# Kernel tuning notes

Measured on AMD Instinct MI355X. Metric: run time of the kernel, lower is better.

## Reference

```python
import jax, jax.numpy as jnp
import numpy as np
from jax import lax

T_STEPS = 10       # fixed unroll length in forward (range(10))
TASK = 16          # params['task_size']
FEAT = 256         # input_size - task_size
VOCAB = 128        # params['vocab_size']
SH = 512           # sender_hidden_size
RH = 512           # receiver_hidden_size
ND = 10            # num_digits
B = 16384          # batch_size


def _gru_step(h, x, Wih, Whh, bih, bhh):
    # PyTorch GRU/GRUCell equations. Wih: [3H, In], Whh: [3H, H]
    gi = x @ Wih.T + bih
    gh = h @ Whh.T + bhh
    ir, iz, inn = jnp.split(gi, 3, axis=-1)
    hr, hz, hn = jnp.split(gh, 3, axis=-1)
    r = jax.nn.sigmoid(ir + hr)
    z = jax.nn.sigmoid(iz + hz)
    n = jnp.tanh(inn + r * hn)
    return (1.0 - z) * n + z * h


def setup_inputs() -> dict:
    key = jax.random.key(0)
    ks = jax.random.split(key, 16)
    s = 0.05
    x = jax.random.normal(ks[0], (B, TASK + FEAT), jnp.float32)
    u = jax.random.uniform(ks[1], (T_STEPS, B, VOCAB), jnp.float32, 1e-6, 1.0 - 1e-6)
    gumbel = -jnp.log(-jnp.log(u))  # standard Gumbel noise, fixed for determinism
    inp = {
        "x": x,
        "gumbel": gumbel,
        "W_in": jax.random.normal(ks[2], (SH, FEAT), jnp.float32) * s,
        "b_in": jnp.zeros((SH,), jnp.float32),
        "Wih_s": jax.random.normal(ks[3], (3 * SH, VOCAB), jnp.float32) * s,
        "Whh_s": jax.random.normal(ks[4], (3 * SH, SH), jnp.float32) * s,
        "bih_s": jnp.zeros((3 * SH,), jnp.float32),
        "bhh_s": jnp.zeros((3 * SH,), jnp.float32),
        "W_sp": jax.random.normal(ks[5], (VOCAB, SH), jnp.float32) * s,
        "b_sp": jnp.zeros((VOCAB,), jnp.float32),
        "Wih_r": jax.random.normal(ks[6], (3 * RH, VOCAB), jnp.float32) * s,
        "Whh_r": jax.random.normal(ks[7], (3 * RH, RH), jnp.float32) * s,
        "bih_r": jnp.zeros((3 * RH,), jnp.float32),
        "bhh_r": jnp.zeros((3 * RH,), jnp.float32),
        "W_c": jax.random.normal(ks[8], (ND, RH + TASK), jnp.float32) * s,
        "b_c": jnp.zeros((ND,), jnp.float32),
    }
    return inp


def _forward(x, gumbel, W_in, b_in, Wih_s, Whh_s, bih_s, bhh_s, W_sp, b_sp,
             Wih_r, Whh_r, bih_r, bhh_r, W_c, b_c):
    feats = x[:, TASK:]
    task = x[:, :TASK]
    h0 = jnp.tanh(feats @ W_in.T + b_in)                      # [B, SH]
    inp0 = jnp.zeros((x.shape[0], VOCAB), x.dtype)

    def sender_step(carry, g):
        h, w = carry
        h = _gru_step(h, w, Wih_s, Whh_s, bih_s, bhh_s)
        logits = h @ W_sp.T + b_sp
        y_soft = jax.nn.softmax(logits + g, axis=-1)          # gumbel_softmax, tau=1
        onehot = jax.nn.one_hot(jnp.argmax(y_soft, axis=-1), VOCAB, dtype=y_soft.dtype)
        y = onehot + y_soft - lax.stop_gradient(y_soft)       # hard straight-through
        return (h, lax.stop_gradient(y)), y                   # input_word = y.detach()

    (_, _), output_words = lax.scan(sender_step, (h0, inp0), gumbel)  # [10, B, V]

    # cumulative stop-token masking: once argmax==0 at step i-1, zero all steps >= i
    words = jnp.argmax(output_words, axis=2)                  # [10, B]
    nz = (words != 0).astype(output_words.dtype)
    alive = jnp.concatenate(
        [jnp.ones((1, words.shape[1]), output_words.dtype), jnp.cumprod(nz[:-1], axis=0)],
        axis=0)                                               # [10, B]
    masked = output_words * alive[:, :, None]

    # receiver GRU, zero initial hidden, return final hidden
    hr0 = jnp.zeros((x.shape[0], RH), x.dtype)

    def recv_step(h, w):
        h = _gru_step(h, w, Wih_r, Whh_r, bih_r, bhh_r)
        return h, None

    h_n, _ = lax.scan(recv_step, hr0, masked)                 # [B, RH]
    score = jnp.concatenate([h_n, task], axis=1) @ W_c.T + b_c  # [B, ND]
    return score


def reference(x, gumbel, W_in, b_in, Wih_s, Whh_s, bih_s, bhh_s, W_sp, b_sp,
              Wih_r, Whh_r, bih_r, bhh_r, W_c, b_c):
    return _forward(x, gumbel, W_in, b_in, Wih_s, Whh_s, bih_s, bhh_s, W_sp, b_sp,
                    Wih_r, Whh_r, bih_r, bhh_r, W_c, b_c)
```

## Files before the change

### kernel.cpp

```cpp
#include <hip/hip_runtime.h>
#include <math.h>

#define NB 16384
#define NT 10

typedef _Float16 f16;
typedef f16 f16x8 __attribute__((ext_vector_type(8)));
typedef f16 f16x4 __attribute__((ext_vector_type(4)));
typedef float f32x4 __attribute__((ext_vector_type(4)));

__device__ __forceinline__ float sigm(float v) { return 1.0f / (1.0f + expf(-v)); }
__device__ __forceinline__ float sigm_fast(float v) {
    return __builtin_amdgcn_rcpf(1.0f + __expf(-v));
}
__device__ __forceinline__ float tanh_fast(float v) {
    return 1.0f - 2.0f * __builtin_amdgcn_rcpf(1.0f + __expf(2.0f * v));
}

__device__ __forceinline__ void async_cp16(const f16* g, f16* l) {
    __builtin_amdgcn_global_load_lds(
        (const __attribute__((address_space(1))) unsigned int*)g,
        (__attribute__((address_space(3))) unsigned int*)l, 16, 0, 0);
}

__global__ __launch_bounds__(256) void h0_kernel(
    const float* __restrict__ x, const float* __restrict__ W,
    const float* __restrict__ bias, f16* __restrict__ h_hi, f16* __restrict__ h_lo)
{
    __shared__ __align__(16) float As[32][128];
    __shared__ __align__(16) float Ws[32][64];
    const int t = threadIdx.x;
    const int tx = t & 15, ty = t >> 4;
    const int mBase = blockIdx.x * 128, nBase = blockIdx.y * 64;
    const int kq = (t & 7) * 4, r8 = t >> 3;

    float4 acc[8];
    #pragma unroll
    for (int mi = 0; mi < 8; ++mi) acc[mi] = make_float4(0.f, 0.f, 0.f, 0.f);

    const float* aPtr = x + (size_t)(mBase + r8) * 272 + 16 + kq;
    const float* wPtr = W + (size_t)(nBase + r8) * 256 + kq;

    for (int kb = 0; kb < 8; ++kb) {
        const int k0 = kb * 32;
        __syncthreads();
        #pragma unroll
        for (int i = 0; i < 4; ++i) {
            float4 v = *(const float4*)(aPtr + (size_t)(i * 32) * 272 + k0);
            const int row = r8 + i * 32;
            const float vv[4] = {v.x, v.y, v.z, v.w};
            #pragma unroll
            for (int j = 0; j < 4; ++j) As[kq + j][row ^ ((kq + j) & 28)] = vv[j];
        }
        #pragma unroll
        for (int i = 0; i < 2; ++i) {
            float4 v = *(const float4*)(wPtr + (size_t)(i * 32) * 256 + k0);
            const int row = r8 + i * 32;
            const float vv[4] = {v.x, v.y, v.z, v.w};
            #pragma unroll
            for (int j = 0; j < 4; ++j) Ws[kq + j][row ^ ((kq + j) & 28)] = vv[j];
        }
        __syncthreads();
        #pragma unroll 8
        for (int k = 0; k < 32; ++k) {
            const int s = k & 28;
            float4 a0 = *(const float4*)&As[k][(ty * 8) ^ s];
            float4 a1 = *(const float4*)&As[k][((ty * 8) + 4) ^ s];
            float4 bb = *(const float4*)&Ws[k][(tx * 4) ^ s];
            const float am[8] = {a0.x, a0.y, a0.z, a0.w, a1.x, a1.y, a1.z, a1.w};
            #pragma unroll
            for (int mi = 0; mi < 8; ++mi) {
                acc[mi].x += am[mi] * bb.x; acc[mi].y += am[mi] * bb.y;
                acc[mi].z += am[mi] * bb.z; acc[mi].w += am[mi] * bb.w;
            }
        }
    }
    const int j0 = nBase + tx * 4;
    const int kg = j0 >> 3, jo = j0 & 7;
    const float4 b4 = *(const float4*)&bias[j0];
    #pragma unroll
    for (int mi = 0; mi < 8; ++mi) {
        const int row = mBase + ty * 8 + mi;
        float o[4];
        o[0] = tanhf(acc[mi].x + b4.x); o[1] = tanhf(acc[mi].y + b4.y);
        o[2] = tanhf(acc[mi].z + b4.z); o[3] = tanhf(acc[mi].w + b4.w);
        f16x4 hi4, lo4;
        #pragma unroll
        for (int c = 0; c < 4; ++c) {
            f16 hv = (f16)o[c];
            hi4[c] = hv;
            lo4[c] = (f16)(o[c] - (float)hv);
        }
        *(f16x4*)&h_hi[((size_t)kg * NB + row) * 8 + jo] = hi4;
        *(f16x4*)&h_lo[((size_t)kg * NB + row) * 8 + jo] = lo4;
    }
}

__global__ __launch_bounds__(256) void wsplit_kernel(
    const float* __restrict__ W, f16* __restrict__ whi, f16* __restrict__ wlo, int rows)
{
    const int u = blockIdx.x * 256 + threadIdx.x;
    const int kg = u / rows, row = u - kg * rows;
    const float* s = W + (size_t)row * 512 + kg * 8;
    f16x8 hi8, lo8;
    #pragma unroll
    for (int i = 0; i < 8; ++i) {
        float v = s[i];
        f16 hv = (f16)v;
        hi8[i] = hv;
        lo8[i] = (f16)(v - (float)hv);
    }
    *(f16x8*)&whi[(size_t)u * 8] = hi8;
    *(f16x8*)&wlo[(size_t)u * 8] = lo8;
}

__global__ __launch_bounds__(256) void wihT_kernel(
    const float* __restrict__ Wih, float* __restrict__ WihT)
{
    const int u = blockIdx.x * 256 + threadIdx.x;
    const int w = u / 1536, c = u - w * 1536;
    WihT[u] = Wih[(size_t)c * 128 + w];
}

#define INIT_SP() { \
    _Pragma("unroll") \
    for (int i = 0; i < NST; ++i) { \
        const int u = i * 256 + t; \
        const f16* src; \
        if (PURE) { \
            if (u < 512) { \
                src = hc_hi + ((size_t)(u >> 7) * NB + m0 + (u & 127)) * 8; \
            } else { \
                const int w = u - 512; \
                src = w_hi + ((size_t)((w >> 6) & 3) * 1536 + (w >> 8) * 512 + n0 + (w & 63)) * 8; \
            } \
        } else { \
            if (u < 1024) { \
                const int v = u & 511; \
                const f16* hp = (u < 512) ? hc_hi : hc_lo; \
                src = hp + ((size_t)(v >> 7) * NB + m0 + (v & 127)) * 8; \
            } else { \
                const int v = u - 1024; \
                const f16* wp = (v < 768) ? w_hi : w_lo; \
                const int w = (v < 768) ? v : v - 768; \
                src = wp + ((size_t)((w >> 6) & 3) * 1536 + (w >> 8) * 512 + n0 + (w & 63)) * 8; \
            } \
        } \
        sp[i] = src; \
    } \
}
#define STAGE(buf_) { \
    f16* lb_ = lds + ((size_t)(buf_) * UNITS + wbase) * 8; \
    _Pragma("unroll") \
    for (int i = 0; i < NST; ++i) { \
        async_cp16(sp[i], lb_ + (size_t)i * 256 * 8); \
        sp[i] += (i < HCNT) ? (size_t)NB * 32 : (size_t)49152; \
    } \
}

template <int HZERO, int PURE>
__global__ __launch_bounds__(256, 2) void fused_gru(
    const f16* __restrict__ hc_hi, const f16* __restrict__ hc_lo,
    f16* __restrict__ hn_hi, f16* __restrict__ hn_lo,
    const f16* __restrict__ w_hi, const f16* __restrict__ w_lo,
    const float* __restrict__ WihT,
    const float* __restrict__ bih, const float* __restrict__ bhh,
    const int* __restrict__ wsel)
{
    constexpr int UNITS = PURE ? 1280 : 2560;
    constexpr int NST = PURE ? 5 : 10;
    constexpr int HCNT = PURE ? 2 : 4;
    __shared__ __align__(16) f16 lds[2 * UNITS * 8];
    const int t = threadIdx.x;
    const int lane = t & 63, wave = t >> 6;
    const int wm = wave >> 1, wn = wave & 1;
    const int nid = (blockIdx.x & 7) * (NB / 128 * 8 / 8) + (blockIdx.x >> 3);
    const int m0 = (nid >> 3) * 128;
    const int n0 = (nid & 7) * 64;
    const int wbase = t & 192;

    const f32x4 z4 = {0.f, 0.f, 0.f, 0.f};
    f32x4 acc[3][4][2];
    #pragma unroll
    for (int g = 0; g < 3; ++g)
        #pragma unroll
        for (int mi = 0; mi < 4; ++mi)
            #pragma unroll
            for (int ni = 0; ni < 2; ++ni) acc[g][mi][ni] = z4;

    if (!HZERO) {
        const int asel = ((lane >> 4) << 7) + wm * 64 + (lane & 15);
        const int bsel = ((lane >> 4) << 6) + wn * 32 + (lane & 15);
        constexpr int B0 = PURE ? 512 : 1024;

        const f16* sp[NST];
        INIT_SP();
        STAGE(0);
        asm volatile("s_waitcnt vmcnt(0)" ::: "memory");
        __syncthreads();

        for (int kb = 0; kb < 16; ++kb) {
            if (kb < 15) STAGE((kb + 1) & 1);

            const f16* lb = lds + (size_t)(kb & 1) * UNITS * 8;
            f16x8 ah[4], al[4];
            #pragma unroll
            for (int mi = 0; mi < 4; ++mi) {
                ah[mi] = *(const f16x8*)&lb[(size_t)(asel + mi * 16) * 8];
                if (!PURE) al[mi] = *(const f16x8*)&lb[(size_t)(512 + asel + mi * 16) * 8];
            }
            #pragma unroll
            for (int g = 0; g < 3; ++g) {
                f16x8 bh[2], bl[2];
                #pragma unroll
                for (int ni = 0; ni < 2; ++ni) {
                    bh[ni] = *(const f16x8*)&lb[(size_t)(B0 + g * 256 + bsel + ni * 16) * 8];
                    if (!PURE) bl[ni] = *(const f16x8*)&lb[(size_t)(1792 + g * 256 + bsel + ni * 16) * 8];
                }
                #pragma unroll
                for (int mi = 0; mi < 4; ++mi)
                    #pragma unroll
                    for (int ni = 0; ni < 2; ++ni) {
                        acc[g][mi][ni] = __builtin_amdgcn_mfma_f32_16x16x32_f16(ah[mi], bh[ni], acc[g][mi][ni], 0, 0, 0);
                        if (!PURE) {
                            acc[g][mi][ni] = __builtin_amdgcn_mfma_f32_16x16x32_f16(ah[mi], bl[ni], acc[g][mi][ni], 0, 0, 0);
                            acc[g][mi][ni] = __builtin_amdgcn_mfma_f32_16x16x32_f16(al[mi], bh[ni], acc[g][mi][ni], 0, 0, 0);
                        }
                    }
            }
            __syncthreads();
        }
    }

    const int colb = n0 + wn * 32 + (lane & 15);
    const int rowb = m0 + wm * 64 + ((lane >> 4) << 2);
    int wd[16];
    #pragma unroll
    for (int mi = 0; mi < 4; ++mi)
        #pragma unroll
        for (int j = 0; j < 4; ++j)
            wd[mi * 4 + j] = wsel ? wsel[rowb + mi * 16 + j] : -1;

    #pragma unroll
    for (int ni = 0; ni < 2; ++ni) {
        const int col = colb + ni * 16;
        const float b_r = bih[col], b_z = bih[512 + col], b_n = bih[1024 + col];
        const float c_r = bhh[col], c_z = bhh[512 + col], c_n = bhh[1024 + col];
        const size_t cbase = (size_t)(col >> 3) * NB * 8 + (col & 7);
        #pragma unroll
        for (int mi = 0; mi < 4; ++mi) {
            #pragma unroll
            for (int j = 0; j < 4; ++j) {
                const int r = rowb + mi * 16 + j;
                const int word = wd[mi * 4 + j];
                float wir = 0.f, wiz = 0.f, win = 0.f;
                if (word >= 0) {
                    const float* wt = WihT + (size_t)word * 1536 + col;
                    wir = wt[0]; wiz = wt[512]; win = wt[1024];
                }
                const size_t idx = cbase + (size_t)r * 8;
                float hold = 0.f;
                if (!HZERO) {
                    hold = (float)hc_hi[idx];
                    if (!PURE) hold += (float)hc_lo[idx];
                }
                const float ra = wir + b_r + acc[0][mi][ni][j] + c_r;
                const float za = wiz + b_z + acc[1][mi][ni][j] + c_z;
                const float rr = PURE ? sigm_fast(ra) : sigm(ra);
                const float zz = PURE ? sigm_fast(za) : sigm(za);
                const float na = win + b_n + rr * (acc[2][mi][ni][j] + c_n);
                const float nn = PURE ? tanh_fast(na) : tanhf(na);
                const float hv = (1.f - zz) * nn + zz * hold;
                const f16 hh = (f16)hv;
                hn_hi[idx] = hh;
                if (!PURE) hn_lo[idx] = (f16)(hv - (float)hh);
            }
        }
    }
}

__global__ __launch_bounds__(256, 2) void argmax_mfma(
    const f16* __restrict__ h_hi, const f16* __restrict__ h_lo,
    const f16* __restrict__ wsp_hi, const f16* __restrict__ wsp_lo,
    const float* __restrict__ bsp, const float* __restrict__ gum,
    int* __restrict__ wout)
{
    __shared__ __align__(16) f16 lds[2 * 1536 * 8];
    const int t = threadIdx.x;
    const int lane = t & 63, wave = t >> 6;
    const int mBase = blockIdx.x * 64;

    const f32x4 z4 = {0.f, 0.f, 0.f, 0.f};
    f32x4 acc[8];
    #pragma unroll
    for (int nf = 0; nf < 8; ++nf) acc[nf] = z4;

    const f16* sp[6];
    sp[0] = h_hi   + ((size_t)(t >> 6) * NB + mBase + (t & 63)) * 8;
    sp[1] = h_lo   + ((size_t)(t >> 6) * NB + mBase + (t & 63)) * 8;
    sp[2] = wsp_hi + ((size_t)(t >> 7) * 128 + (t & 127)) * 8;
    sp[3] = wsp_hi + ((size_t)(2 + (t >> 7)) * 128 + (t & 127)) * 8;
    sp[4] = wsp_lo + ((size_t)(t >> 7) * 128 + (t & 127)) * 8;
    sp[5] = wsp_lo + ((size_t)(2 + (t >> 7)) * 128 + (t & 127)) * 8;

    f16x8 st[6];
    #pragma unroll
    for (int i = 0; i < 6; ++i) {
        st[i] = *(const f16x8*)sp[i];
        sp[i] += (i < 2) ? (size_t)NB * 32 : (size_t)4096;
    }

    const int aselU = (lane >> 4) * 64 + wave * 16 + (lane & 15);
    const int bselU = 512 + (lane >> 4) * 128 + (lane & 15);

    for (int kb = 0; kb < 16; ++kb) {
        f16* lb = lds + (size_t)(kb & 1) * 1536 * 8;
        #pragma unroll
        for (int i = 0; i < 6; ++i)
            *(f16x8*)&lb[(size_t)(i * 256 + t) * 8] = st[i];
        __syncthreads();
        if (kb < 15) {
            #pragma unroll
            for (int i = 0; i < 6; ++i) {
                st[i] = *(const f16x8*)sp[i];
                sp[i] += (i < 2) ? (size_t)NB * 32 : (size_t)4096;
            }
        }

        f16x8 ah = *(const f16x8*)&lb[(size_t)aselU * 8];
        f16x8 al = *(const f16x8*)&lb[(size_t)(256 + aselU) * 8];
        #pragma unroll
        for (int nf = 0; nf < 8; ++nf) {
            f16x8 bh = *(const f16x8*)&lb[(size_t)(bselU + nf * 16) * 8];
            f16x8 bl = *(const f16x8*)&lb[(size_t)(512 + bselU + nf * 16) * 8];
            acc[nf] = __builtin_amdgcn_mfma_f32_16x16x32_f16(ah, bh, acc[nf], 0, 0, 0);
            acc[nf] = __builtin_amdgcn_mfma_f32_16x16x32_f16(ah, bl, acc[nf], 0, 0, 0);
            acc[nf] = __builtin_amdgcn_mfma_f32_16x16x32_f16(al, bh, acc[nf], 0, 0, 0);
        }
    }

    float bv[4];
    int bi[4];
    #pragma unroll
    for (int j = 0; j < 4; ++j) { bv[j] = -1e30f; bi[j] = 0; }
    const int rw0 = mBase + wave * 16 + ((lane >> 4) << 2);
    #pragma unroll
    for (int nf = 0; nf < 8; ++nf) {
        const int col = (lane & 15) + nf * 16;
        const float bb = bsp[col];
        #pragma unroll
        for (int j = 0; j < 4; ++j) {
            const float v = acc[nf][j] + bb + gum[(size_t)(rw0 + j) * 128 + col];
            if (v > bv[j] || (v == bv[j] && col < bi[j])) { bv[j] = v; bi[j] = col; }
        }
    }
    #pragma unroll
    for (int j = 0; j < 4; ++j) {
        #pragma unroll
        for (int off = 1; off <= 8; off <<= 1) {
            const float ov = __shfl_xor(bv[j], off, 64);
            const int oi = __shfl_xor(bi[j], off, 64);
            if (ov > bv[j] || (ov == bv[j] && oi < bi[j])) { bv[j] = ov; bi[j] = oi; }
        }
        if ((lane & 15) == 0) wout[rw0 + j] = bi[j];
    }
}

__global__ __launch_bounds__(256) void eff_kernel(
    const int* __restrict__ words, int* __restrict__ eff)
{
    const int b = blockIdx.x * 256 + threadIdx.x;
    int alive = 1;
    #pragma unroll
    for (int t = 0; t < NT; ++t) {
        const int w = words[(size_t)t * NB + b];
        eff[(size_t)t * NB + b] = alive ? w : -1;
        alive = alive & (w != 0);
    }
}

__global__ __launch_bounds__(256) void score_kernel(
    const f16* __restrict__ h_hi,
    const float* __restrict__ x, const float* __restrict__ Wc,
    const float* __restrict__ bc, float* __restrict__ out)
{
    __shared__ float Wcs[10][528];
    const int t = threadIdx.x;
    for (int q = t; q < 1320; q += 256)
        *(float4*)&(((float*)Wcs)[q * 4]) = *(const float4*)&Wc[q * 4];
    __syncthreads();

    const int row = blockIdx.x * 256 + t;
    float acc[10];
    #pragma unroll
    for (int d = 0; d < 10; ++d) acc[d] = 0.f;

    for (int kg = 0; kg < 64; ++kg) {
        f16x8 vh = *(const f16x8*)&h_hi[((size_t)kg * NB + row) * 8];
        #pragma unroll
        for (int i = 0; i < 8; ++i) {
            const float v = (float)vh[i];
            #pragma unroll
            for (int d = 0; d < 10; ++d) acc[d] += v * Wcs[d][kg * 8 + i];
        }
    }
    #pragma unroll
    for (int j = 0; j < 16; ++j) {
        const float tv = x[(size_t)row * 272 + j];
        #pragma unroll
        for (int d = 0; d < 10; ++d) acc[d] += tv * Wcs[d][512 + j];
    }
    #pragma unroll
    for (int d = 0; d < 10; ++d) out[(size_t)row * 10 + d] = acc[d] + bc[d];
}

extern "C" void kernel_launch(void* const* d_in, const int* in_sizes, int n_in,
                              void* d_out, int out_size, void* d_ws, size_t ws_size,
                              hipStream_t stream) {
    const float* x      = (const float*)d_in[0];
    const float* gumbel = (const float*)d_in[1];
    const float* W_in   = (const float*)d_in[2];
    const float* b_in   = (const float*)d_in[3];
    const float* Wih_s  = (const float*)d_in[4];
    const float* Whh_s  = (const float*)d_in[5];
    const float* bih_s  = (const float*)d_in[6];
    const float* bhh_s  = (const float*)d_in[7];
    const float* W_sp   = (const float*)d_in[8];
    const float* b_sp   = (const float*)d_in[9];
    const float* Wih_r  = (const float*)d_in[10];
    const float* Whh_r  = (const float*)d_in[11];
    const float* bih_r  = (const float*)d_in[12];
    const float* bhh_r  = (const float*)d_in[13];
    const float* W_c    = (const float*)d_in[14];
    const float* b_c    = (const float*)d_in[15];
    float* out = (float*)d_out;

    char* base = (char*)d_ws;
    f16* S_hi[2], *S_lo[2];
    S_hi[0] = (f16*)(base);
    S_lo[0] = (f16*)(base + 16777216);
    S_hi[1] = (f16*)(base + 33554432);
    S_lo[1] = (f16*)(base + 50331648);
    f16* R0 = (f16*)(base);
    f16* R1 = (f16*)(base + 16777216);
    f16* ws_s_hi = (f16*)(base + 67108864);
    f16* ws_s_lo = (f16*)(base + 68681728);
    f16* ws_r_hi = (f16*)(base + 70254592);
    f16* ws_r_lo = (f16*)(base + 71827456);
    float* wihT_s = (float*)(base + 73400320);
    float* wihT_r = (float*)(base + 74186752);
    int* words   = (int*)(base + 74973184);
    int* eff     = (int*)(base + 75628544);
    f16* wsp_hi  = (f16*)(base + 76283904);
    f16* wsp_lo  = (f16*)(base + 76414976);

    const dim3 blk(256);
    const dim3 gFus(NB / 128 * 8);

    wsplit_kernel<<<dim3(384), blk, 0, stream>>>(Whh_s, ws_s_hi, ws_s_lo, 1536);
    wsplit_kernel<<<dim3(384), blk, 0, stream>>>(Whh_r, ws_r_hi, ws_r_lo, 1536);
    wsplit_kernel<<<dim3(32), blk, 0, stream>>>(W_sp, wsp_hi, wsp_lo, 128);
    wihT_kernel<<<dim3(768), blk, 0, stream>>>(Wih_s, wihT_s);
    wihT_kernel<<<dim3(768), blk, 0, stream>>>(Wih_r, wihT_r);

    h0_kernel<<<dim3(NB / 128, 8), blk, 0, stream>>>(x, W_in, b_in, S_hi[0], S_lo[0]);
    int cur = 0;

    for (int t = 0; t < NT; ++t) {
        const int* wprev = (t == 0) ? (const int*)nullptr : (words + (size_t)(t - 1) * NB);
        const int nxt = cur ^ 1;
        fused_gru<0, 0><<<gFus, blk, 0, stream>>>(
            S_hi[cur], S_lo[cur], S_hi[nxt], S_lo[nxt],
            ws_s_hi, ws_s_lo, wihT_s, bih_s, bhh_s, wprev);
        cur = nxt;
        argmax_mfma<<<dim3(NB / 64), blk, 0, stream>>>(
            S_hi[cur], S_lo[cur], wsp_hi, wsp_lo,
            b_sp, gumbel + (size_t)t * NB * 128, words + (size_t)t * NB);
    }
    eff_kernel<<<dim3(NB / 256), blk, 0, stream>>>(words, eff);

    fused_gru<1, 1><<<gFus, blk, 0, stream>>>(
        R1, R1, R0, R0, ws_r_hi, ws_r_lo, wihT_r, bih_r, bhh_r, eff);
    for (int t = 1; t < NT; ++t) {
        f16* rin  = (t & 1) ? R0 : R1;
        f16* rout = (t & 1) ? R1 : R0;
        fused_gru<0, 1><<<gFus, blk, 0, stream>>>(
            rin, rin, rout, rout, ws_r_hi, ws_r_lo, wihT_r, bih_r, bhh_r,
            eff + (size_t)t * NB);
    }

    score_kernel<<<dim3(NB / 256), blk, 0, stream>>>(R1, x, W_c, b_c, out);
}
```

Baseline: 1.516 ms.

## Move h0 projection to split-fp16 MFMA and use faster sender activations

Replaces the scalar fp32 FMA GEMM for the initial hidden state with an MFMA kernel. Both the input features and W_in are first split into hi/lo fp16 parts in new preprocessing kernels, and the product uses three MFMA terms to keep near-fp32 accuracy. It also swaps the sender GRU's accurate expf/tanhf for __expf-based sigmoid and tanh. The extra split kernels add memory traffic and launches, and the faster transcendentals may slightly change argmax decisions.

New measurement: 1.460 ms. 3.7% less time.

```diff
diff --git a/kernel.cpp b/kernel.cpp
--- a/kernel.cpp
+++ b/kernel.cpp
@@ -9,7 +9,8 @@
 typedef f16 f16x4 __attribute__((ext_vector_type(4)));
 typedef float f32x4 __attribute__((ext_vector_type(4)));
 
-__device__ __forceinline__ float sigm(float v) { return 1.0f / (1.0f + expf(-v)); }
+__device__ __forceinline__ float sigm_mid(float v) { return 1.0f / (1.0f + __expf(-v)); }
+__device__ __forceinline__ float tanh_mid(float v) { return 1.0f - 2.0f / (1.0f + __expf(2.0f * v)); }
 __device__ __forceinline__ float sigm_fast(float v) {
     return __builtin_amdgcn_rcpf(1.0f + __expf(-v));
 }
@@ -23,85 +24,13 @@
         (__attribute__((address_space(3))) unsigned int*)l, 16, 0, 0);
 }
 
-__global__ __launch_bounds__(256) void h0_kernel(
-    const float* __restrict__ x, const float* __restrict__ W,
-    const float* __restrict__ bias, f16* __restrict__ h_hi, f16* __restrict__ h_lo)
-{
-    __shared__ __align__(16) float As[32][128];
-    __shared__ __align__(16) float Ws[32][64];
-    const int t = threadIdx.x;
-    const int tx = t & 15, ty = t >> 4;
-    const int mBase = blockIdx.x * 128, nBase = blockIdx.y * 64;
-    const int kq = (t & 7) * 4, r8 = t >> 3;
-
-    float4 acc[8];
-    #pragma unroll
-    for (int mi = 0; mi < 8; ++mi) acc[mi] = make_float4(0.f, 0.f, 0.f, 0.f);
-
-    const float* aPtr = x + (size_t)(mBase + r8) * 272 + 16 + kq;
-    const float* wPtr = W + (size_t)(nBase + r8) * 256 + kq;
-
-    for (int kb = 0; kb < 8; ++kb) {
-        const int k0 = kb * 32;
-        __syncthreads();
-        #pragma unroll
-        for (int i = 0; i < 4; ++i) {
-            float4 v = *(const float4*)(aPtr + (size_t)(i * 32) * 272 + k0);
-            const int row = r8 + i * 32;
-            const float vv[4] = {v.x, v.y, v.z, v.w};
-            #pragma unroll
-            for (int j = 0; j < 4; ++j) As[kq + j][row ^ ((kq + j) & 28)] = vv[j];
-        }
-        #pragma unroll
-        for (int i = 0; i < 2; ++i) {
-            float4 v = *(const float4*)(wPtr + (size_t)(i * 32) * 256 + k0);
-            const int row = r8 + i * 32;
-            const float vv[4] = {v.x, v.y, v.z, v.w};
-            #pragma unroll
-            for (int j = 0; j < 4; ++j) Ws[kq + j][row ^ ((kq + j) & 28)] = vv[j];
-        }
-        __syncthreads();
-        #pragma unroll 8
-        for (int k = 0; k < 32; ++k) {
-            const int s = k & 28;
-            float4 a0 = *(const float4*)&As[k][(ty * 8) ^ s];
-            float4 a1 = *(const float4*)&As[k][((ty * 8) + 4) ^ s];
-            float4 bb = *(const float4*)&Ws[k][(tx * 4) ^ s];
-            const float am[8] = {a0.x, a0.y, a0.z, a0.w, a1.x, a1.y, a1.z, a1.w};
-            #pragma unroll
-            for (int mi = 0; mi < 8; ++mi) {
-                acc[mi].x += am[mi] * bb.x; acc[mi].y += am[mi] * bb.y;
-                acc[mi].z += am[mi] * bb.z; acc[mi].w += am[mi] * bb.w;
-            }
-        }
-    }
-    const int j0 = nBase + tx * 4;
-    const int kg = j0 >> 3, jo = j0 & 7;
-    const float4 b4 = *(const float4*)&bias[j0];
-    #pragma unroll
-    for (int mi = 0; mi < 8; ++mi) {
-        const int row = mBase + ty * 8 + mi;
-        float o[4];
-        o[0] = tanhf(acc[mi].x + b4.x); o[1] = tanhf(acc[mi].y + b4.y);
-        o[2] = tanhf(acc[mi].z + b4.z); o[3] = tanhf(acc[mi].w + b4.w);
-        f16x4 hi4, lo4;
-        #pragma unroll
-        for (int c = 0; c < 4; ++c) {
-            f16 hv = (f16)o[c];
-            hi4[c] = hv;
-            lo4[c] = (f16)(o[c] - (float)hv);
-        }
-        *(f16x4*)&h_hi[((size_t)kg * NB + row) * 8 + jo] = hi4;
-        *(f16x4*)&h_lo[((size_t)kg * NB + row) * 8 + jo] = lo4;
-    }
-}
-
 __global__ __launch_bounds__(256) void wsplit_kernel(
-    const float* __restrict__ W, f16* __restrict__ whi, f16* __restrict__ wlo, int rows)
+    const float* __restrict__ W, f16* __restrict__ whi, f16* __restrict__ wlo,
+    int rows, int kstride)
 {
     const int u = blockIdx.x * 256 + threadIdx.x;
     const int kg = u / rows, row = u - kg * rows;
-    const float* s = W + (size_t)row * 512 + kg * 8;
+    const float* s = W + (size_t)row * kstride + kg * 8;
     f16x8 hi8, lo8;
     #pragma unroll
     for (int i = 0; i < 8; ++i) {
@@ -114,12 +43,137 @@
     *(f16x8*)&wlo[(size_t)u * 8] = lo8;
 }
 
+__global__ __launch_bounds__(256) void xsplit_kernel(
+    const float* __restrict__ x, f16* __restrict__ xhi, f16* __restrict__ xlo)
+{
+    const int u = blockIdx.x * 256 + threadIdx.x;
+    const int kg = u >> 14, row = u & (NB - 1);
+    const float* s = x + (size_t)row * 272 + 16 + kg * 8;
+    f16x8 hi8, lo8;
+    #pragma unroll
+    for (int i = 0; i < 8; ++i) {
+        float v = s[i];
+        f16 hv = (f16)v;
+        hi8[i] = hv;
+        lo8[i] = (f16)(v - (float)hv);
+    }
+    *(f16x8*)&xhi[(size_t)u * 8] = hi8;
+    *(f16x8*)&xlo[(size_t)u * 8] = lo8;
+}
+
 __global__ __launch_bounds__(256) void wihT_kernel(
     const float* __restrict__ Wih, float* __restrict__ WihT)
 {
     const int u = blockIdx.x * 256 + threadIdx.x;
     const int w = u / 1536, c = u - w * 1536;
     WihT[u] = Wih[(size_t)c * 128 + w];
+}
+
+__global__ __launch_bounds__(256, 2) void h0_mfma(
+    const f16* __restrict__ xs_hi, const f16* __restrict__ xs_lo,
+    const f16* __restrict__ win_hi, const f16* __restrict__ win_lo,
+    const float* __restrict__ bias, f16* __restrict__ h_hi, f16* __restrict__ h_lo)
+{
+    constexpr int UNITS = 1536;
+    __shared__ __align__(16) f16 lds[2 * UNITS * 8];
+    const int t = threadIdx.x;
+    const int lane = t & 63, wave = t >> 6;
+    const int wm = wave >> 1, wn = wave & 1;
+    const int nid = (blockIdx.x & 7) * 128 + (blockIdx.x >> 3);
+    const int m0 = (nid >> 3) * 128;
+    const int n0 = (nid & 7) * 64;
+    const int wbase = t & 192;
+
+    const f32x4 z4 = {0.f, 0.f, 0.f, 0.f};
+    f32x4 acc[4][2];
+    #pragma unroll
+    for (int mi = 0; mi < 4; ++mi)
+        #pragma unroll
+        for (int ni = 0; ni < 2; ++ni) acc[mi][ni] = z4;
+
+    const int asel = ((lane >> 4) << 7) + wm * 64 + (lane & 15);
+    const int bsel = ((lane >> 4) << 6) + wn * 32 + (lane & 15);
+
+    const f16* sp[6];
+    #pragma unroll
+    for (int i = 0; i < 6; ++i) {
+        const int u = i * 256 + t;
+        const f16* src;
+        if (u < 512) {
+            src = xs_hi + ((size_t)(u >> 7) * NB + m0 + (u & 127)) * 8;
+        } else if (u < 1024) {
+            const int v = u - 512;
+            src = xs_lo + ((size_t)(v >> 7) * NB + m0 + (v & 127)) * 8;
+        } else if (u < 1280) {
+            const int v = u - 1024;
+            src = win_hi + ((size_t)(v >> 6) * 512 + n0 + (v & 63)) * 8;
+        } else {
+            const int v = u - 1280;
+            src = win_lo + ((size_t)(v >> 6) * 512 + n0 + (v & 63)) * 8;
+        }
+        sp[i] = src;
+    }
+
+    #define H0_STAGE(buf_) { \
+        f16* lb_ = lds + ((size_t)(buf_) * UNITS + wbase) * 8; \
+        _Pragma("unroll") \
+        for (int i = 0; i < 6; ++i) { \
+            async_cp16(sp[i], lb_ + (size_t)i * 256 * 8); \
+            sp[i] += (i < 4) ? (size_t)NB * 32 : (size_t)16384; \
+        } \
+    }
+
+    H0_STAGE(0);
+    asm volatile("s_waitcnt vmcnt(0)" ::: "memory");
+    __syncthreads();
+
+    for (int kb = 0; kb < 8; ++kb) {
+        if (kb < 7) H0_STAGE((kb + 1) & 1);
+
+        const f16* lb = lds + (size_t)(kb & 1) * UNITS * 8;
+        f16x8 ah[4], al[4];
+        #pragma unroll
+        for (int mi = 0; mi < 4; ++mi) {
+            ah[mi] = *(const f16x8*)&lb[(size_t)(asel + mi * 16) * 8];
+            al[mi] = *(const f16x8*)&lb[(size_t)(512 + asel + mi * 16) * 8];
+        }
+        f16x8 bh[2], bl[2];
+        #pragma unroll
+        for (int ni = 0; ni < 2; ++ni) {
+            bh[ni] = *(const f16x8*)&lb[(size_t)(1024 + bsel + ni * 16) * 8];
+            bl[ni] = *(const f16x8*)&lb[(size_t)(1280 + bsel + ni * 16) * 8];
+        }
+        #pragma unroll
+        for (int mi = 0; mi < 4; ++mi)
+            #pragma unroll
+            for (int ni = 0; ni < 2; ++ni) {
+                acc[mi][ni] = __builtin_amdgcn_mfma_f32_16x16x32_f16(ah[mi], bh[ni], acc[mi][ni], 0, 0, 0);
+                acc[mi][ni] = __builtin_amdgcn_mfma_f32_16x16x32_f16(ah[mi], bl[ni], acc[mi][ni], 0, 0, 0);
+                acc[mi][ni] = __builtin_amdgcn_mfma_f32_16x16x32_f16(al[mi], bh[ni], acc[mi][ni], 0, 0, 0);
+            }
+        __syncthreads();
+    }
+
+    const int colb = n0 + wn * 32 + (lane & 15);
+    const int rowb = m0 + wm * 64 + ((lane >> 4) << 2);
+    #pragma unroll
+    for (int ni = 0; ni < 2; ++ni) {
+        const int col = colb + ni * 16;
+        const float bb = bias[col];
+        const size_t cbase = (size_t)(col >> 3) * NB * 8 + (col & 7);
+        #pragma unroll
+        for (int mi = 0; mi < 4; ++mi) {
+            #pragma unroll
+            for (int j = 0; j < 4; ++j) {
+                const int r = rowb + mi * 16 + j;
+                const float o = tanhf(acc[mi][ni][j] + bb);
+                const f16 hh = (f16)o;
+                const size_t idx = cbase + (size_t)r * 8;
+                h_hi[idx] = hh;
+                h_lo[idx] = (f16)(o - (float)hh);
+            }
+        }
+    }
 }
 
 #define INIT_SP() { \
@@ -174,7 +228,7 @@
     const int t = threadIdx.x;
     const int lane = t & 63, wave = t >> 6;
     const int wm = wave >> 1, wn = wave & 1;
-    const int nid = (blockIdx.x & 7) * (NB / 128 * 8 / 8) + (blockIdx.x >> 3);
+    const int nid = (blockIdx.x & 7) * 128 + (blockIdx.x >> 3);
     const int m0 = (nid >> 3) * 128;
     const int n0 = (nid & 7) * 64;
     const int wbase = t & 192;
@@ -266,10 +320,10 @@
                 }
                 const float ra = wir + b_r + acc[0][mi][ni][j] + c_r;
                 const float za = wiz + b_z + acc[1][mi][ni][j] + c_z;
-                const float rr = PURE ? sigm_fast(ra) : sigm(ra);
-                const float zz = PURE ? sigm_fast(za) : sigm(za);
+                const float rr = PURE ? sigm_fast(ra) : sigm_mid(ra);
+                const float zz = PURE ? sigm_fast(za) : sigm_mid(za);
                 const float na = win + b_n + rr * (acc[2][mi][ni][j] + c_n);
-                const float nn = PURE ? tanh_fast(na) : tanhf(na);
+                const float nn = PURE ? tanh_fast(na) : tanh_mid(na);
                 const float hv = (1.f - zz) * nn + zz * hold;
                 const f16 hh = (f16)hv;
                 hn_hi[idx] = hh;
@@ -453,17 +507,23 @@
     int* eff     = (int*)(base + 75628544);
     f16* wsp_hi  = (f16*)(base + 76283904);
     f16* wsp_lo  = (f16*)(base + 76414976);
+    f16* xs_hi   = (f16*)(base + 76546048);
+    f16* xs_lo   = (f16*)(base + 84934656);
+    f16* win_hi  = (f16*)(base + 93323264);
+    f16* win_lo  = (f16*)(base + 93585408);
 
     const dim3 blk(256);
     const dim3 gFus(NB / 128 * 8);
 
-    wsplit_kernel<<<dim3(384), blk, 0, stream>>>(Whh_s, ws_s_hi, ws_s_lo, 1536);
-    wsplit_kernel<<<dim3(384), blk, 0, stream>>>(Whh_r, ws_r_hi, ws_r_lo, 1536);
-    wsplit_kernel<<<dim3(32), blk, 0, stream>>>(W_sp, wsp_hi, wsp_lo, 128);
+    wsplit_kernel<<<dim3(384), blk, 0, stream>>>(Whh_s, ws_s_hi, ws_s_lo, 1536, 512);
+    wsplit_kernel<<<dim3(384), blk, 0, stream>>>(Whh_r, ws_r_hi, ws_r_lo, 1536, 512);
+    wsplit_kernel<<<dim3(32), blk, 0, stream>>>(W_sp, wsp_hi, wsp_lo, 128, 512);
+    wsplit_kernel<<<dim3(64), blk, 0, stream>>>(W_in, win_hi, win_lo, 512, 256);
+    xsplit_kernel<<<dim3(2048), blk, 0, stream>>>(x, xs_hi, xs_lo);
     wihT_kernel<<<dim3(768), blk, 0, stream>>>(Wih_s, wihT_s);
     wihT_kernel<<<dim3(768), blk, 0, stream>>>(Wih_r, wihT_r);
 
-    h0_kernel<<<dim3(NB / 128, 8), blk, 0, stream>>>(x, W_in, b_in, S_hi[0], S_lo[0]);
+    h0_mfma<<<gFus, blk, 0, stream>>>(xs_hi, xs_lo, win_hi, win_lo, b_in, S_hi[0], S_lo[0]);
     int cur = 0;
 
     for (int t = 0; t < NT; ++t) {
```
